# Performance work log

Measured on AMD Instinct MI355X. Metric: run time of the kernel, lower is better.

Reference implementation:

```python
import jax, jax.numpy as jnp
import numpy as np

EMB = 1024
FF = 1024
EPS = 1e-5

def _layernorm(x, g, b):
    mu = jnp.mean(x, axis=-1, keepdims=True)
    var = jnp.mean((x - mu) ** 2, axis=-1, keepdims=True)
    return (x - mu) * jax.lax.rsqrt(var + EPS) * g + b

def setup_inputs() -> dict:
    key = jax.random.key(0)
    ks = jax.random.split(key, 12)
    s = 1.0 / np.sqrt(EMB)
    x = jax.random.normal(ks[0], (4, 2048, EMB), dtype=jnp.float32)
    Wq = jax.random.normal(ks[1], (EMB, EMB), dtype=jnp.float32) * s
    bq = jnp.zeros((EMB,), jnp.float32)
    Wk = jax.random.normal(ks[2], (EMB, EMB), dtype=jnp.float32) * s
    bk = jnp.zeros((EMB,), jnp.float32)
    Wv = jax.random.normal(ks[3], (EMB, EMB), dtype=jnp.float32) * s
    bv = jnp.zeros((EMB,), jnp.float32)
    Wo = jax.random.normal(ks[4], (EMB, EMB), dtype=jnp.float32) * s
    bo = jnp.zeros((EMB,), jnp.float32)
    W1 = jax.random.normal(ks[5], (EMB, FF), dtype=jnp.float32) * s
    b1 = jnp.zeros((FF,), jnp.float32)
    W2 = jax.random.normal(ks[6], (FF, EMB), dtype=jnp.float32) * (1.0 / np.sqrt(FF))
    b2 = jnp.zeros((EMB,), jnp.float32)
    g1 = jnp.ones((EMB,), jnp.float32); be1 = jnp.zeros((EMB,), jnp.float32)
    g2 = jnp.ones((EMB,), jnp.float32); be2 = jnp.zeros((EMB,), jnp.float32)
    return {"x": x, "Wq": Wq, "bq": bq, "Wk": Wk, "bk": bk, "Wv": Wv, "bv": bv,
            "Wo": Wo, "bo": bo, "W1": W1, "b1": b1, "W2": W2, "b2": b2,
            "g1": g1, "be1": be1, "g2": g2, "be2": be2}

def reference(x, Wq, bq, Wk, bk, Wv, bv, Wo, bo, W1, b1, W2, b2, g1, be1, g2, be2):
    # pre-norm single-head self-attention + residual + FFN (dropout = identity, eval)
    xn = _layernorm(x, g1, be1)
    q = xn @ Wq + bq
    k = xn @ Wk + bk
    v = xn @ Wv + bv
    scores = jnp.einsum('bse,bte->bst', q, k) / jnp.sqrt(jnp.float32(EMB))
    w = jax.nn.softmax(scores, axis=-1)              # [B,S,S]
    attn = jnp.einsum('bst,bte->bse', w, v) @ Wo + bo
    x2 = x + attn
    xn2 = _layernorm(x2, g2, be2)
    ff = jax.nn.relu(xn2 @ W1 + b1) @ W2 + b2
    out = x2 + ff
    return (out, w)
```

## Files before the change

### kernel.cpp

```cpp
#include <hip/hip_runtime.h>

typedef __attribute__((ext_vector_type(8))) __bf16 bf16x8;
typedef __attribute__((ext_vector_type(4))) float f32x4;
typedef __attribute__((ext_vector_type(8))) ushort ushort8;

#define GLP(p) ((const __attribute__((address_space(1))) void*)(p))
#define LDP(p) ((__attribute__((address_space(3))) void*)(p))

__device__ __forceinline__ ushort f2b(float f) {
  union { float f; uint u; } c; c.f = f;
  uint u = c.u;
  uint r = (u + 0x7fffu + ((u >> 16) & 1u)) >> 16;
  return (ushort)r;
}

__device__ __forceinline__ float block_reduce_sum(float v, float* sm) {
#pragma unroll
  for (int off = 1; off < 64; off <<= 1) v += __shfl_xor(v, off);
  const int wave = threadIdx.x >> 6, lane = threadIdx.x & 63;
  __syncthreads();
  if (lane == 0) sm[wave] = v;
  __syncthreads();
  return sm[0] + sm[1] + sm[2] + sm[3];
}

__global__ __launch_bounds__(256) void wtrans6_kernel(
    const float* __restrict__ W0, const float* __restrict__ W1,
    const float* __restrict__ W2, const float* __restrict__ W3,
    const float* __restrict__ W4, const float* __restrict__ W5,
    ushort* __restrict__ T0, ushort* __restrict__ T1, ushort* __restrict__ T2,
    ushort* __restrict__ T3, ushort* __restrict__ T4, ushort* __restrict__ T5) {
  __shared__ float tile[32][33];
  const float* Ws[6] = {W0, W1, W2, W3, W4, W5};
  ushort* Ts[6] = {T0, T1, T2, T3, T4, T5};
  const float* W = Ws[blockIdx.z];
  ushort* Wt = Ts[blockIdx.z];
  const int K = 1024, N = 1024;
  const int n0 = blockIdx.x * 32, k0 = blockIdx.y * 32;
  const int tx = threadIdx.x, ty = threadIdx.y;
#pragma unroll
  for (int i = 0; i < 32; i += 8)
    tile[ty + i][tx] = W[(long)(k0 + ty + i) * N + n0 + tx];
  __syncthreads();
#pragma unroll
  for (int i = 0; i < 32; i += 8)
    Wt[(long)(n0 + ty + i) * K + k0 + tx] = f2b(tile[tx][ty + i]);
}

__global__ __launch_bounds__(256) void layernorm_kernel(
    const float* __restrict__ x, const float* __restrict__ g,
    const float* __restrict__ be, ushort* __restrict__ out) {
  __shared__ float sm[4];
  const long row = blockIdx.x;
  const float4 v = reinterpret_cast<const float4*>(x + row * 1024)[threadIdx.x];
  float s = v.x + v.y + v.z + v.w;
  s = block_reduce_sum(s, sm);
  const float mu = s * (1.0f / 1024.0f);
  const float dx = v.x - mu, dy = v.y - mu, dz = v.z - mu, dw = v.w - mu;
  float s2 = dx * dx + dy * dy + dz * dz + dw * dw;
  s2 = block_reduce_sum(s2, sm);
  const float rstd = rsqrtf(s2 * (1.0f / 1024.0f) + 1e-5f);
  const float4 gg = reinterpret_cast<const float4*>(g)[threadIdx.x];
  const float4 bb = reinterpret_cast<const float4*>(be)[threadIdx.x];
  ushort4 o;
  o.x = f2b(dx * rstd * gg.x + bb.x);
  o.y = f2b(dy * rstd * gg.y + bb.y);
  o.z = f2b(dz * rstd * gg.z + bb.z);
  o.w = f2b(dw * rstd * gg.w + bb.w);
  reinterpret_cast<ushort4*>(out + row * 1024)[threadIdx.x] = o;
}

__global__ __launch_bounds__(256) void softmax_kernel(
    float* __restrict__ s, ushort* __restrict__ wb) {
  __shared__ float sm[4];
  const long row = blockIdx.x;
  float4* r4 = reinterpret_cast<float4*>(s + row * 2048);
  float4 v0 = r4[threadIdx.x * 2];
  float4 v1 = r4[threadIdx.x * 2 + 1];
  float m = fmaxf(fmaxf(fmaxf(v0.x, v0.y), fmaxf(v0.z, v0.w)),
                  fmaxf(fmaxf(v1.x, v1.y), fmaxf(v1.z, v1.w)));
#pragma unroll
  for (int off = 1; off < 64; off <<= 1) m = fmaxf(m, __shfl_xor(m, off));
  const int wave = threadIdx.x >> 6, lane = threadIdx.x & 63;
  if (lane == 0) sm[wave] = m;
  __syncthreads();
  m = fmaxf(fmaxf(sm[0], sm[1]), fmaxf(sm[2], sm[3]));
  v0.x = expf(v0.x - m); v0.y = expf(v0.y - m);
  v0.z = expf(v0.z - m); v0.w = expf(v0.w - m);
  v1.x = expf(v1.x - m); v1.y = expf(v1.y - m);
  v1.z = expf(v1.z - m); v1.w = expf(v1.w - m);
  float sum = v0.x + v0.y + v0.z + v0.w + v1.x + v1.y + v1.z + v1.w;
  sum = block_reduce_sum(sum, sm);
  const float inv = 1.0f / sum;
  v0.x *= inv; v0.y *= inv; v0.z *= inv; v0.w *= inv;
  v1.x *= inv; v1.y *= inv; v1.z *= inv; v1.w *= inv;
  r4[threadIdx.x * 2] = v0;
  r4[threadIdx.x * 2 + 1] = v1;
  ushort8 o;
  o[0] = f2b(v0.x); o[1] = f2b(v0.y); o[2] = f2b(v0.z); o[3] = f2b(v0.w);
  o[4] = f2b(v1.x); o[5] = f2b(v1.y); o[6] = f2b(v1.z); o[7] = f2b(v1.w);
  *reinterpret_cast<ushort8*>(wb + row * 2048 + threadIdx.x * 8) = o;
}

#define EP_BF16 1
#define EP_F32 2
#define EP_BIAS 4
#define EP_RELU 8
#define EP_SCALE 16
#define EP_RESID 32
#define EP_TRANS 64

template <int FLAGS>
__global__ __launch_bounds__(512) void gemm_bt(
    const ushort* __restrict__ A, const ushort* __restrict__ Bt,
    float* __restrict__ Cf, ushort* __restrict__ Cb,
    const float* __restrict__ bias, const float* __restrict__ resid,
    int M, int N, int K, float scale, long sA, long sB, long sC) {
  A += (long)blockIdx.z * sA;
  Bt += (long)blockIdx.z * sB;
  const long coff = (long)blockIdx.z * sC;
  const int tileN = blockIdx.x * 128, tileM = blockIdx.y * 128;
  const int tid = threadIdx.x, lane = tid & 63, wid = tid >> 6;
  const int wm = wid >> 2, wn = wid & 3;
  __shared__ alignas(16) ushort As[2][128][32];
  __shared__ alignas(16) ushort Bs[2][128][32];
  f32x4 acc[4][2] = {};

  const int srow = wid * 16 + (lane >> 2);
  const int scol = (lane & 3) * 8;
  const ushort* aP = A + (long)(tileM + srow) * K + scol;
  const ushort* bP = Bt + (long)(tileN + srow) * K + scol;

#define STAGE(buf, kk)                                                                   \
  do {                                                                                   \
    __builtin_amdgcn_global_load_lds(GLP(aP + (kk)), LDP(&As[buf][wid * 16][0]), 16, 0,  \
                                     0);                                                 \
    __builtin_amdgcn_global_load_lds(GLP(bP + (kk)), LDP(&Bs[buf][wid * 16][0]), 16, 0,  \
                                     0);                                                 \
  } while (0)

  STAGE(0, 0);
  __syncthreads();
  int cur = 0;
  for (int kk = 0; kk < K; kk += 32) {
    const int nxt = cur ^ 1;
    if (kk + 32 < K) STAGE(nxt, kk + 32);
    bf16x8 a[4], b[2];
#pragma unroll
    for (int m = 0; m < 4; ++m)
      a[m] = *reinterpret_cast<const bf16x8*>(
          &As[cur][wm * 64 + m * 16 + (lane & 15)][(lane >> 4) * 8]);
#pragma unroll
    for (int n = 0; n < 2; ++n)
      b[n] = *reinterpret_cast<const bf16x8*>(
          &Bs[cur][wn * 32 + n * 16 + (lane & 15)][(lane >> 4) * 8]);
#pragma unroll
    for (int m = 0; m < 4; ++m)
#pragma unroll
      for (int n = 0; n < 2; ++n)
        acc[m][n] = __builtin_amdgcn_mfma_f32_16x16x32_bf16(a[m], b[n], acc[m][n], 0, 0, 0);
    __syncthreads();
    cur = nxt;
  }
#undef STAGE

  const int row0 = tileM + wm * 64 + ((lane >> 4) << 2);
  const int col0 = tileN + wn * 32 + (lane & 15);
#pragma unroll
  for (int n = 0; n < 2; ++n) {
    const int col = col0 + n * 16;
    const float bv = (FLAGS & EP_BIAS) ? bias[col] : 0.0f;
#pragma unroll
    for (int m = 0; m < 4; ++m) {
#pragma unroll
      for (int i = 0; i < 4; ++i) {
        const int row = row0 + m * 16 + i;
        float v = acc[m][n][i];
        if (FLAGS & EP_SCALE) v *= scale;
        v += bv;
        if (FLAGS & EP_RELU) v = fmaxf(v, 0.0f);
        if (FLAGS & EP_RESID) v += resid[coff + (long)row * N + col];
        if (FLAGS & EP_F32) Cf[coff + (long)row * N + col] = v;
        if (FLAGS & EP_BF16) {
          if (FLAGS & EP_TRANS)
            Cb[coff + (long)col * M + row] = f2b(v);
          else
            Cb[coff + (long)row * N + col] = f2b(v);
        }
      }
    }
  }
}

__global__ __launch_bounds__(512) void gemm_qkv(
    const ushort* __restrict__ A, const ushort* __restrict__ Bt,
    ushort* __restrict__ Cq, ushort* __restrict__ Ck, ushort* __restrict__ Cv,
    const float* __restrict__ bq, const float* __restrict__ bk,
    const float* __restrict__ bv, int M, int N, int K) {
  const int tileN = blockIdx.x * 128, tileM = blockIdx.y * 128;
  const int tid = threadIdx.x, lane = tid & 63, wid = tid >> 6;
  const int wm = wid >> 2, wn = wid & 3;
  __shared__ alignas(16) ushort As[2][128][32];
  __shared__ alignas(16) ushort Bs[2][128][32];
  f32x4 acc[4][2] = {};

  const int srow = wid * 16 + (lane >> 2);
  const int scol = (lane & 3) * 8;
  const ushort* aP = A + (long)(tileM + srow) * K + scol;
  const ushort* bP = Bt + (long)(tileN + srow) * K + scol;

#define STAGE(buf, kk)                                                                   \
  do {                                                                                   \
    __builtin_amdgcn_global_load_lds(GLP(aP + (kk)), LDP(&As[buf][wid * 16][0]), 16, 0,  \
                                     0);                                                 \
    __builtin_amdgcn_global_load_lds(GLP(bP + (kk)), LDP(&Bs[buf][wid * 16][0]), 16, 0,  \
                                     0);                                                 \
  } while (0)

  STAGE(0, 0);
  __syncthreads();
  int cur = 0;
  for (int kk = 0; kk < K; kk += 32) {
    const int nxt = cur ^ 1;
    if (kk + 32 < K) STAGE(nxt, kk + 32);
    bf16x8 a[4], b[2];
#pragma unroll
    for (int m = 0; m < 4; ++m)
      a[m] = *reinterpret_cast<const bf16x8*>(
          &As[cur][wm * 64 + m * 16 + (lane & 15)][(lane >> 4) * 8]);
#pragma unroll
    for (int n = 0; n < 2; ++n)
      b[n] = *reinterpret_cast<const bf16x8*>(
          &Bs[cur][wn * 32 + n * 16 + (lane & 15)][(lane >> 4) * 8]);
#pragma unroll
    for (int m = 0; m < 4; ++m)
#pragma unroll
      for (int n = 0; n < 2; ++n)
        acc[m][n] = __builtin_amdgcn_mfma_f32_16x16x32_bf16(a[m], b[n], acc[m][n], 0, 0, 0);
    __syncthreads();
    cur = nxt;
  }
#undef STAGE

  const int seg = tileN >> 10;
  const float* bias = (seg == 0) ? bq : (seg == 1) ? bk : bv;
  const int row0 = tileM + wm * 64 + ((lane >> 4) << 2);
  const int col0 = tileN + wn * 32 + (lane & 15);
#pragma unroll
  for (int n = 0; n < 2; ++n) {
    const int col = col0 + n * 16;
    const int bcol = col & 1023;
    const float bvv = bias[bcol];
#pragma unroll
    for (int m = 0; m < 4; ++m) {
#pragma unroll
      for (int i = 0; i < 4; ++i) {
        const int row = row0 + m * 16 + i;
        const float v = acc[m][n][i] + bvv;
        if (seg == 0) {
          Cq[(long)row * 1024 + bcol] = f2b(v);
        } else if (seg == 1) {
          Ck[(long)row * 1024 + bcol] = f2b(v);
        } else {
          Cv[((long)(row >> 11) * 1024 + bcol) * 2048 + (row & 2047)] = f2b(v);
        }
      }
    }
  }
}

extern "C" void kernel_launch(void* const* d_in, const int* in_sizes, int n_in,
                              void* d_out, int out_size, void* d_ws, size_t ws_size,
                              hipStream_t stream) {
  const int B = 4, S = 2048, E = 1024, FFD = 1024;
  const long MS = (long)B * S;
  const float* x   = (const float*)d_in[0];
  const float* Wq  = (const float*)d_in[1];
  const float* bq  = (const float*)d_in[2];
  const float* Wk  = (const float*)d_in[3];
  const float* bk  = (const float*)d_in[4];
  const float* Wv  = (const float*)d_in[5];
  const float* bv  = (const float*)d_in[6];
  const float* Wo  = (const float*)d_in[7];
  const float* bo  = (const float*)d_in[8];
  const float* W1  = (const float*)d_in[9];
  const float* b1  = (const float*)d_in[10];
  const float* W2  = (const float*)d_in[11];
  const float* b2  = (const float*)d_in[12];
  const float* g1  = (const float*)d_in[13];
  const float* be1 = (const float*)d_in[14];
  const float* g2  = (const float*)d_in[15];
  const float* be2 = (const float*)d_in[16];

  float* out  = (float*)d_out;
  float* wout = out + MS * E;

  ushort* xnA = (ushort*)d_ws;
  ushort* qB  = xnA + MS * E;
  ushort* kC  = qB + MS * E;
  ushort* vTD = kC + MS * E;
  ushort* wE  = vTD + MS * E;
  float*  x2F = (float*)(wE + (long)B * S * S);
  ushort* wts = (ushort*)(x2F + MS * E);
  ushort* WqT = wts;
  ushort* WkT = WqT + (long)E * E;
  ushort* WvT = WkT + (long)E * E;
  ushort* WoT = WvT + (long)E * E;
  ushort* W1T = WoT + (long)E * E;
  ushort* W2T = W1T + (long)E * FFD;

  hipLaunchKernelGGL(wtrans6_kernel, dim3(E / 32, E / 32, 6), dim3(32, 8), 0, stream,
                     Wq, Wk, Wv, Wo, W1, W2, WqT, WkT, WvT, WoT, W1T, W2T);

  hipLaunchKernelGGL(layernorm_kernel, dim3(MS), dim3(256), 0, stream, x, g1, be1, xnA);

  hipLaunchKernelGGL(gemm_qkv, dim3(3 * E / 128, MS / 128, 1), dim3(512), 0, stream,
                     xnA, WqT, qB, kC, vTD, bq, bk, bv, (int)MS, 3 * E, E);

  hipLaunchKernelGGL((gemm_bt<EP_F32 | EP_SCALE>), dim3(S / 128, S / 128, B), dim3(512), 0,
                     stream, qB, kC, wout, (ushort*)nullptr, (const float*)nullptr,
                     (const float*)nullptr, S, S, E, 0.03125f, (long)S * E, (long)S * E,
                     (long)S * S);

  hipLaunchKernelGGL(softmax_kernel, dim3(B * S), dim3(256), 0, stream, wout, wE);

  hipLaunchKernelGGL((gemm_bt<EP_BF16>), dim3(E / 128, S / 128, B), dim3(512), 0, stream,
                     wE, vTD, (float*)nullptr, qB, (const float*)nullptr,
                     (const float*)nullptr, S, E, S, 1.0f, (long)S * S, (long)E * S,
                     (long)S * E);

  hipLaunchKernelGGL((gemm_bt<EP_F32 | EP_BIAS | EP_RESID>), dim3(E / 128, MS / 128, 1),
                     dim3(512), 0, stream, qB, WoT, x2F, (ushort*)nullptr, bo, x,
                     (int)MS, E, E, 1.0f, 0L, 0L, 0L);

  hipLaunchKernelGGL(layernorm_kernel, dim3(MS), dim3(256), 0, stream, x2F, g2, be2, xnA);

  hipLaunchKernelGGL((gemm_bt<EP_BF16 | EP_BIAS | EP_RELU>), dim3(FFD / 128, MS / 128, 1),
                     dim3(512), 0, stream, xnA, W1T, (float*)nullptr, kC, b1,
                     (const float*)nullptr, (int)MS, FFD, E, 1.0f, 0L, 0L, 0L);

  hipLaunchKernelGGL((gemm_bt<EP_F32 | EP_BIAS | EP_RESID>), dim3(E / 128, MS / 128, 1),
                     dim3(512), 0, stream, kC, W2T, out, (ushort*)nullptr, b2, x2F,
                     (int)MS, E, FFD, 1.0f, 0L, 0L, 0L);
}
```

Measured before the change: 351.1 us.

## Remap GEMM tiles across XCDs and double the K step per barrier

Adds an XCD-aware remapping of block IDs to output tiles, so consecutive tiles land on the same chiplet and share L2. Each main-loop iteration now covers 64 K values using four LDS slots instead of 32 with two. This halves the number of __syncthreads per GEMM and keeps a larger prefetch in flight. LDS use per block doubles, and the remap assumes the tile count divides by 8.

```diff
diff --git a/kernel.cpp b/kernel.cpp
--- a/kernel.cpp
+++ b/kernel.cpp
@@ -12,6 +12,15 @@
   uint u = c.u;
   uint r = (u + 0x7fffu + ((u >> 16) & 1u)) >> 16;
   return (ushort)r;
+}
+
+__device__ __forceinline__ void xcd_tiles(int& tileN, int& tileM) {
+  const int gx = gridDim.x;
+  const int nwg = gx * gridDim.y;
+  int id = blockIdx.x + gx * blockIdx.y;
+  id = (id & 7) * (nwg >> 3) + (id >> 3);
+  tileN = (id % gx) * 128;
+  tileM = (id / gx) * 128;
 }
 
 __device__ __forceinline__ float block_reduce_sum(float v, float* sm) {
@@ -119,11 +128,12 @@
   A += (long)blockIdx.z * sA;
   Bt += (long)blockIdx.z * sB;
   const long coff = (long)blockIdx.z * sC;
-  const int tileN = blockIdx.x * 128, tileM = blockIdx.y * 128;
+  int tileN, tileM;
+  xcd_tiles(tileN, tileM);
   const int tid = threadIdx.x, lane = tid & 63, wid = tid >> 6;
   const int wm = wid >> 2, wn = wid & 3;
-  __shared__ alignas(16) ushort As[2][128][32];
-  __shared__ alignas(16) ushort Bs[2][128][32];
+  __shared__ alignas(16) ushort As[4][128][32];
+  __shared__ alignas(16) ushort Bs[4][128][32];
   f32x4 acc[4][2] = {};
 
   const int srow = wid * 16 + (lane >> 2);
@@ -131,34 +141,42 @@
   const ushort* aP = A + (long)(tileM + srow) * K + scol;
   const ushort* bP = Bt + (long)(tileN + srow) * K + scol;
 
-#define STAGE(buf, kk)                                                                   \
+#define STAGE(slot, kk)                                                                  \
   do {                                                                                   \
-    __builtin_amdgcn_global_load_lds(GLP(aP + (kk)), LDP(&As[buf][wid * 16][0]), 16, 0,  \
+    __builtin_amdgcn_global_load_lds(GLP(aP + (kk)), LDP(&As[slot][wid * 16][0]), 16, 0, \
                                      0);                                                 \
-    __builtin_amdgcn_global_load_lds(GLP(bP + (kk)), LDP(&Bs[buf][wid * 16][0]), 16, 0,  \
+    __builtin_amdgcn_global_load_lds(GLP(bP + (kk)), LDP(&Bs[slot][wid * 16][0]), 16, 0, \
                                      0);                                                 \
   } while (0)
 
   STAGE(0, 0);
+  STAGE(1, 32);
   __syncthreads();
   int cur = 0;
-  for (int kk = 0; kk < K; kk += 32) {
-    const int nxt = cur ^ 1;
-    if (kk + 32 < K) STAGE(nxt, kk + 32);
-    bf16x8 a[4], b[2];
-#pragma unroll
-    for (int m = 0; m < 4; ++m)
-      a[m] = *reinterpret_cast<const bf16x8*>(
-          &As[cur][wm * 64 + m * 16 + (lane & 15)][(lane >> 4) * 8]);
-#pragma unroll
-    for (int n = 0; n < 2; ++n)
-      b[n] = *reinterpret_cast<const bf16x8*>(
-          &Bs[cur][wn * 32 + n * 16 + (lane & 15)][(lane >> 4) * 8]);
-#pragma unroll
-    for (int m = 0; m < 4; ++m)
+  for (int kk = 0; kk < K; kk += 64) {
+    const int nxt = cur ^ 2;
+    if (kk + 64 < K) {
+      STAGE(nxt, kk + 64);
+      STAGE(nxt + 1, kk + 96);
+    }
+#pragma unroll
+    for (int u = 0; u < 2; ++u) {
+      const int sl = cur + u;
+      bf16x8 a[4], b[2];
+#pragma unroll
+      for (int m = 0; m < 4; ++m)
+        a[m] = *reinterpret_cast<const bf16x8*>(
+            &As[sl][wm * 64 + m * 16 + (lane & 15)][(lane >> 4) * 8]);
 #pragma unroll
       for (int n = 0; n < 2; ++n)
-        acc[m][n] = __builtin_amdgcn_mfma_f32_16x16x32_bf16(a[m], b[n], acc[m][n], 0, 0, 0);
+        b[n] = *reinterpret_cast<const bf16x8*>(
+            &Bs[sl][wn * 32 + n * 16 + (lane & 15)][(lane >> 4) * 8]);
+#pragma unroll
+      for (int m = 0; m < 4; ++m)
+#pragma unroll
+        for (int n = 0; n < 2; ++n)
+          acc[m][n] = __builtin_amdgcn_mfma_f32_16x16x32_bf16(a[m], b[n], acc[m][n], 0, 0, 0);
+    }
     __syncthreads();
     cur = nxt;
   }
@@ -197,11 +215,12 @@
     ushort* __restrict__ Cq, ushort* __restrict__ Ck, ushort* __restrict__ Cv,
     const float* __restrict__ bq, const float* __restrict__ bk,
     const float* __restrict__ bv, int M, int N, int K) {
-  const int tileN = blockIdx.x * 128, tileM = blockIdx.y * 128;
+  int tileN, tileM;
+  xcd_tiles(tileN, tileM);
   const int tid = threadIdx.x, lane = tid & 63, wid = tid >> 6;
   const int wm = wid >> 2, wn = wid & 3;
-  __shared__ alignas(16) ushort As[2][128][32];
-  __shared__ alignas(16) ushort Bs[2][128][32];
+  __shared__ alignas(16) ushort As[4][128][32];
+  __shared__ alignas(16) ushort Bs[4][128][32];
   f32x4 acc[4][2] = {};
 
   const int srow = wid * 16 + (lane >> 2);
@@ -209,34 +228,42 @@
   const ushort* aP = A + (long)(tileM + srow) * K + scol;
   const ushort* bP = Bt + (long)(tileN + srow) * K + scol;
 
-#define STAGE(buf, kk)                                                                   \
+#define STAGE(slot, kk)                                                                  \
   do {                                                                                   \
-    __builtin_amdgcn_global_load_lds(GLP(aP + (kk)), LDP(&As[buf][wid * 16][0]), 16, 0,  \
+    __builtin_amdgcn_global_load_lds(GLP(aP + (kk)), LDP(&As[slot][wid * 16][0]), 16, 0, \
                                      0);                                                 \
-    __builtin_amdgcn_global_load_lds(GLP(bP + (kk)), LDP(&Bs[buf][wid * 16][0]), 16, 0,  \
+    __builtin_amdgcn_global_load_lds(GLP(bP + (kk)), LDP(&Bs[slot][wid * 16][0]), 16, 0, \
                                      0);                                                 \
   } while (0)
 
   STAGE(0, 0);
+  STAGE(1, 32);
   __syncthreads();
   int cur = 0;
-  for (int kk = 0; kk < K; kk += 32) {
-    const int nxt = cur ^ 1;
-    if (kk + 32 < K) STAGE(nxt, kk + 32);
-    bf16x8 a[4], b[2];
-#pragma unroll
-    for (int m = 0; m < 4; ++m)
-      a[m] = *reinterpret_cast<const bf16x8*>(
-          &As[cur][wm * 64 + m * 16 + (lane & 15)][(lane >> 4) * 8]);
-#pragma unroll
-    for (int n = 0; n < 2; ++n)
-      b[n] = *reinterpret_cast<const bf16x8*>(
-          &Bs[cur][wn * 32 + n * 16 + (lane & 15)][(lane >> 4) * 8]);
-#pragma unroll
-    for (int m = 0; m < 4; ++m)
+  for (int kk = 0; kk < K; kk += 64) {
+    const int nxt = cur ^ 2;
+    if (kk + 64 < K) {
+      STAGE(nxt, kk + 64);
+      STAGE(nxt + 1, kk + 96);
+    }
+#pragma unroll
+    for (int u = 0; u < 2; ++u) {
+      const int sl = cur + u;
+      bf16x8 a[4], b[2];
+#pragma unroll
+      for (int m = 0; m < 4; ++m)
+        a[m] = *reinterpret_cast<const bf16x8*>(
+            &As[sl][wm * 64 + m * 16 + (lane & 15)][(lane >> 4) * 8]);
 #pragma unroll
       for (int n = 0; n < 2; ++n)
-        acc[m][n] = __builtin_amdgcn_mfma_f32_16x16x32_bf16(a[m], b[n], acc[m][n], 0, 0, 0);
+        b[n] = *reinterpret_cast<const bf16x8*>(
+            &Bs[sl][wn * 32 + n * 16 + (lane & 15)][(lane >> 4) * 8]);
+#pragma unroll
+      for (int m = 0; m < 4; ++m)
+#pragma unroll
+        for (int n = 0; n < 2; ++n)
+          acc[m][n] = __builtin_amdgcn_mfma_f32_16x16x32_bf16(a[m], b[n], acc[m][n], 0, 0, 0);
+    }
     __syncthreads();
     cur = nxt;
   }
```

Result: faster. 329.6 us (-6.1%).
